# Performance work log

Hardware: AMD Instinct MI355X
Metric: run time of the kernel (lower is better)

Reference implementation:

```python
import jax, jax.numpy as jnp
import numpy as np
import math

EMBED_DIM = 1024
NUM_HEADS = 16
HEAD_DIM = EMBED_DIM // NUM_HEADS


def setup_inputs() -> dict:
    key = jax.random.key(0)
    ks = jax.random.split(key, 11)
    B, S, D = 4, 2048, EMBED_DIM
    scale = 1.0 / math.sqrt(D)
    inp = {
        'q': jax.random.normal(ks[0], (B, S, D), dtype=jnp.float32),
        'k': jax.random.normal(ks[1], (B, S, D), dtype=jnp.float32),
        'v': jax.random.normal(ks[2], (B, S, D), dtype=jnp.float32),
        'Wq': jax.random.normal(ks[3], (D, D), dtype=jnp.float32) * scale,
        'bq': jnp.zeros((D,), dtype=jnp.float32),
        'Wk': jax.random.normal(ks[4], (D, D), dtype=jnp.float32) * scale,
        'bk': jnp.zeros((D,), dtype=jnp.float32),
        'Wv': jax.random.normal(ks[5], (D, D), dtype=jnp.float32) * scale,
        'bv': jnp.zeros((D,), dtype=jnp.float32),
        'Wo': jax.random.normal(ks[6], (D, D), dtype=jnp.float32) * scale,
        'bo': jnp.zeros((D,), dtype=jnp.float32),
    }
    return inp


def reference(q, k, v, Wq, bq, Wk, bk, Wv, bv, Wo, bo):
    B, S, D = q.shape
    H, Hd = NUM_HEADS, HEAD_DIM
    # QKV projections (nn.Linear: x @ W.T + b), split into heads -> [B,H,S,Hd]
    qh = (q @ Wq.T + bq).reshape(B, S, H, Hd).transpose(0, 2, 1, 3)
    kh = (k @ Wk.T + bk).reshape(B, S, H, Hd).transpose(0, 2, 1, 3)
    vh = (v @ Wv.T + bv).reshape(B, S, H, Hd).transpose(0, 2, 1, 3)
    # Scaled dot-product attention, full [B,H,S,S] scores as in source
    scores = jnp.einsum('bhqd,bhkd->bhqk', qh, kh) / math.sqrt(Hd)
    probs = jax.nn.softmax(scores, axis=-1)
    attn = jnp.einsum('bhqk,bhkd->bhqd', probs, vh)
    # Merge heads and output projection
    concat = attn.transpose(0, 2, 1, 3).reshape(B, S, D)
    return concat @ Wo.T + bo
```

## Files before the change

kernel.cpp:

```cpp
#include <hip/hip_runtime.h>
#include <hip/hip_bf16.h>
#include <math.h>

#define D_MODEL 1024
#define NHEADS  16
#define HDIM    64
#define BATCH   4
#define SEQ     2048

typedef __attribute__((ext_vector_type(8))) short short8;
typedef __attribute__((ext_vector_type(4))) float f32x4;

__device__ __forceinline__ short bf16_of(float f) {
  __hip_bfloat16 h = __float2bfloat16(f);
  return *reinterpret_cast<short*>(&h);
}

__device__ __forceinline__ unsigned pack2(float lo, float hi) {
  return (unsigned)(unsigned short)bf16_of(lo) |
         ((unsigned)(unsigned short)bf16_of(hi) << 16);
}

__device__ __forceinline__ unsigned cvtpk(float lo, float hi) {
  unsigned r;
  asm("v_cvt_pk_bf16_f32 %0, %1, %2" : "=v"(r) : "v"(lo), "v"(hi));
  return r;
}

__device__ __forceinline__ short8 mk_frag(unsigned a, unsigned b, unsigned c, unsigned d) {
  union { unsigned u[4]; short8 s; } t;
  t.u[0] = a; t.u[1] = b; t.u[2] = c; t.u[3] = d;
  return t.s;
}

__device__ __forceinline__ float fast_exp2(float x) {
  float r;
  asm("v_exp_f32 %0, %1" : "=v"(r) : "v"(x));
  return r;
}

__device__ __forceinline__ void gload16(const void* g, void* l) {
  __builtin_amdgcn_global_load_lds((const __attribute__((address_space(1))) void*)g,
                                   (__attribute__((address_space(3))) void*)l, 16, 0, 0);
}

__global__ __launch_bounds__(256) void cvt7(
    const float* __restrict__ Wq, const float* __restrict__ Wk,
    const float* __restrict__ Wv, const float* __restrict__ Wo,
    const float* __restrict__ q,  const float* __restrict__ k,
    const float* __restrict__ v,
    short* __restrict__ wdst, short* __restrict__ qc,
    short* __restrict__ kc,   short* __restrict__ vc)
{
  const int w = blockIdx.y;
  const float* s;
  short* d;
  int n4;
  if (w < 4) {
    s = (w == 0) ? Wq : (w == 1) ? Wk : (w == 2) ? Wv : Wo;
    d = wdst + (size_t)w * D_MODEL * D_MODEL;
    n4 = D_MODEL * D_MODEL / 4;
  } else {
    s = (w == 4) ? q : (w == 5) ? k : v;
    d = (w == 4) ? qc : (w == 5) ? kc : vc;
    n4 = BATCH * SEQ * D_MODEL / 4;
  }
  int stride = gridDim.x * blockDim.x;
  for (int i = blockIdx.x * blockDim.x + threadIdx.x; i < n4; i += stride) {
    float4 fv = reinterpret_cast<const float4*>(s)[i];
    reinterpret_cast<uint2*>(d)[i] = make_uint2(pack2(fv.x, fv.y), pack2(fv.z, fv.w));
  }
}

__global__ __launch_bounds__(256) void qkv_gemm(
    const short* __restrict__ qc, const short* __restrict__ kc, const short* __restrict__ vc,
    const short* __restrict__ Wqkv,
    const float* __restrict__ bq, const float* __restrict__ bk, const float* __restrict__ bv,
    short* __restrict__ Qb, short* __restrict__ Kb, short* __restrict__ VTb)
{
  const int tid  = threadIdx.x;
  const int lane = tid & 63;
  const int wave = tid >> 6;
  const int Lb  = blockIdx.x + 24 * blockIdx.y;
  const int xcd = Lb & 7;
  const int sl  = Lb >> 3;
  const int bx  = sl % 24;
  const int by  = (sl / 24) * 8 + xcd;

  const int sel = bx >> 3;
  const short* A    = (sel == 0) ? qc : (sel == 1) ? kc : vc;
  const float* bias = (sel == 0) ? bq : (sel == 1) ? bk : bv;
  const int m0  = by * 128;
  const int n0g = bx * 128;
  const int n0  = n0g & 1023;
  const int wm = (wave >> 1) * 64;
  const int wn = (wave & 1) * 64;

  __shared__ short As[128 * 32];
  __shared__ short Bs[128 * 32];

  f32x4 acc[4][4];
#pragma unroll
  for (int m = 0; m < 4; ++m)
#pragma unroll
    for (int n = 0; n < 4; ++n)
      acc[m][n] = (f32x4){0.f, 0.f, 0.f, 0.f};

  for (int k0 = 0; k0 < D_MODEL; k0 += 32) {
#pragma unroll
    for (int i = 0; i < 2; ++i) {
      int t = i * 256 + wave * 64 + lane;
      int row = t >> 2, c8 = (t & 3) * 8;
      gload16(&A[(size_t)(m0 + row) * D_MODEL + k0 + c8],     &As[i * 2048 + wave * 512]);
      gload16(&Wqkv[(size_t)(n0g + row) * D_MODEL + k0 + c8], &Bs[i * 2048 + wave * 512]);
    }
    __syncthreads();

    short8 afr[4], bfr[4];
#pragma unroll
    for (int m = 0; m < 4; ++m)
      afr[m] = *reinterpret_cast<const short8*>(&As[(wm + m * 16 + (lane & 15)) * 32 + (lane >> 4) * 8]);
#pragma unroll
    for (int n = 0; n < 4; ++n)
      bfr[n] = *reinterpret_cast<const short8*>(&Bs[(wn + n * 16 + (lane & 15)) * 32 + (lane >> 4) * 8]);
#pragma unroll
    for (int m = 0; m < 4; ++m)
#pragma unroll
      for (int n = 0; n < 4; ++n)
        acc[m][n] = __builtin_amdgcn_mfma_f32_16x16x32_bf16(afr[m], bfr[n], acc[m][n], 0, 0, 0);
    __syncthreads();
  }

  if (sel < 2) {
    short* Out = (sel == 0) ? Qb : Kb;
#pragma unroll
    for (int n = 0; n < 4; ++n) {
      int col = n0 + wn + n * 16 + (lane & 15);
      float bval = bias[col];
#pragma unroll
      for (int m = 0; m < 4; ++m) {
        int rowb = m0 + wm + m * 16 + (lane >> 4) * 4;
#pragma unroll
        for (int r = 0; r < 4; ++r)
          Out[(size_t)(rowb + r) * D_MODEL + col] = bf16_of(acc[m][n][r] + bval);
      }
    }
  } else {
#pragma unroll
    for (int n = 0; n < 4; ++n) {
      int col = n0 + wn + n * 16 + (lane & 15);
      float bval = bias[col];
      int h = col >> 6, d = col & 63;
#pragma unroll
      for (int m = 0; m < 4; ++m) {
        int s0 = m0 + wm + m * 16 + (lane >> 4) * 4;
        int b = s0 >> 11, sloc = s0 & 2047;
        unsigned lo = pack2(acc[m][n][0] + bval, acc[m][n][1] + bval);
        unsigned hi = pack2(acc[m][n][2] + bval, acc[m][n][3] + bval);
        *reinterpret_cast<uint2*>(
            &VTb[(((size_t)b * NHEADS + h) * HDIM + d) * SEQ + sloc]) = make_uint2(lo, hi);
      }
    }
  }
}

__global__ __launch_bounds__(256) void gemm_out(
    const short* __restrict__ A, const short* __restrict__ Bw,
    const float* __restrict__ bias, float* __restrict__ Out,
    int M, int N, int K)
{
  const int tid  = threadIdx.x;
  const int lane = tid & 63;
  const int wave = tid >> 6;
  const int Lb  = blockIdx.x + 8 * blockIdx.y;
  const int xcd = Lb & 7;
  const int sl  = Lb >> 3;
  const int bx  = sl & 7;
  const int by  = (sl >> 3) * 8 + xcd;
  const int m0 = by * 128;
  const int n0 = bx * 128;
  const int wm = (wave >> 1) * 64;
  const int wn = (wave & 1) * 64;

  __shared__ short As[128 * 32];
  __shared__ short Bs[128 * 32];

  f32x4 acc[4][4];
#pragma unroll
  for (int m = 0; m < 4; ++m)
#pragma unroll
    for (int n = 0; n < 4; ++n)
      acc[m][n] = (f32x4){0.f, 0.f, 0.f, 0.f};

  for (int k0 = 0; k0 < K; k0 += 32) {
#pragma unroll
    for (int i = 0; i < 2; ++i) {
      int t = i * 256 + wave * 64 + lane;
      int row = t >> 2, c8 = (t & 3) * 8;
      gload16(&A[(size_t)(m0 + row) * K + k0 + c8],  &As[i * 2048 + wave * 512]);
      gload16(&Bw[(size_t)(n0 + row) * K + k0 + c8], &Bs[i * 2048 + wave * 512]);
    }
    __syncthreads();

    short8 afr[4], bfr[4];
#pragma unroll
    for (int m = 0; m < 4; ++m)
      afr[m] = *reinterpret_cast<const short8*>(&As[(wm + m * 16 + (lane & 15)) * 32 + (lane >> 4) * 8]);
#pragma unroll
    for (int n = 0; n < 4; ++n)
      bfr[n] = *reinterpret_cast<const short8*>(&Bs[(wn + n * 16 + (lane & 15)) * 32 + (lane >> 4) * 8]);
#pragma unroll
    for (int m = 0; m < 4; ++m)
#pragma unroll
      for (int n = 0; n < 4; ++n)
        acc[m][n] = __builtin_amdgcn_mfma_f32_16x16x32_bf16(afr[m], bfr[n], acc[m][n], 0, 0, 0);
    __syncthreads();
  }

#pragma unroll
  for (int n = 0; n < 4; ++n) {
    int col = n0 + wn + n * 16 + (lane & 15);
    float bval = bias[col];
#pragma unroll
    for (int m = 0; m < 4; ++m) {
      int rowb = m0 + wm + m * 16 + (lane >> 4) * 4;
#pragma unroll
      for (int r = 0; r < 4; ++r)
        Out[(size_t)(rowb + r) * N + col] = acc[m][n][r] + bval;
    }
  }
}

__global__ __launch_bounds__(512) void attn_fwd(
    const short* __restrict__ Q,
    const short* __restrict__ Kg,
    const short* __restrict__ VT,
    short* __restrict__ Oc)
{
  const int tid = threadIdx.x, lane = tid & 63, wave = tid >> 6;
  const int qi = lane & 15, g = lane >> 4;
  const int Lb  = blockIdx.x + 16 * blockIdx.y;
  const int xcd = Lb & 7;
  const int slot = Lb >> 3;
  const int bh  = (slot >> 4) * 8 + xcd;
  const int qblk = slot & 15;
  const int q0 = qblk * 128;
  const int b = bh >> 4, h = bh & 15;

  __shared__ short Ks[2][64][72];
  __shared__ short Vs[2][64][72];

  const float CEXP = 0.18033688f;
  const float SMC  = 14.4269504f;
  const short8 ones = mk_frag(0x3F803F80u, 0x3F803F80u, 0x3F803F80u, 0x3F803F80u);

  short8 qfr[2];
  {
    int qrow = q0 + wave * 16 + qi;
    const short* qp = &Q[((size_t)b * SEQ + qrow) * D_MODEL + h * HDIM + g * 8];
    qfr[0] = *reinterpret_cast<const short8*>(qp);
    qfr[1] = *reinterpret_cast<const short8*>(qp + 32);
  }

  const size_t kbase = ((size_t)b * SEQ) * D_MODEL + h * HDIM;
  const size_t vbase = ((size_t)bh * HDIM) * SEQ;

  f32x4 o[4], o_l;
#pragma unroll
  for (int db = 0; db < 4; ++db) o[db] = (f32x4){0.f, 0.f, 0.f, 0.f};
  o_l = (f32x4){0.f, 0.f, 0.f, 0.f};

  {
    int row = tid >> 3, sub = tid & 7;
    *reinterpret_cast<uint4*>(&Ks[0][row][sub * 8]) =
        *reinterpret_cast<const uint4*>(&Kg[kbase + (size_t)row * D_MODEL + sub * 8]);
    uint4 vv = *reinterpret_cast<const uint4*>(&VT[vbase + (size_t)row * SEQ + sub * 8]);
    int posA = 32 * (sub >> 2) + 16 * (sub & 1) + 4 * ((sub >> 1) & 1);
    *reinterpret_cast<uint2*>(&Vs[0][row][posA])     = make_uint2(vv.x, vv.y);
    *reinterpret_cast<uint2*>(&Vs[0][row][posA + 8]) = make_uint2(vv.z, vv.w);
  }
  __syncthreads();

  for (int t = 0; t < SEQ / 64; ++t) {
    const int cur = t & 1;
    const bool more = (t + 1) < SEQ / 64;
    const int row = tid >> 3, sub = tid & 7;
    uint4 kreg, vreg;
    if (more) {
      int k0 = (t + 1) * 64;
      kreg = *reinterpret_cast<const uint4*>(&Kg[kbase + (size_t)(k0 + row) * D_MODEL + sub * 8]);
      vreg = *reinterpret_cast<const uint4*>(&VT[vbase + (size_t)row * SEQ + k0 + sub * 8]);
    }

    f32x4 st[4];
    __builtin_amdgcn_s_setprio(1);
#pragma unroll
    for (int n = 0; n < 4; ++n) {
      short8 a0 = *reinterpret_cast<const short8*>(&Ks[cur][n * 16 + qi][g * 8]);
      short8 a1 = *reinterpret_cast<const short8*>(&Ks[cur][n * 16 + qi][32 + g * 8]);
      f32x4 z = (f32x4){0.f, 0.f, 0.f, 0.f};
      z = __builtin_amdgcn_mfma_f32_16x16x32_bf16(a0, qfr[0], z, 0, 0, 0);
      z = __builtin_amdgcn_mfma_f32_16x16x32_bf16(a1, qfr[1], z, 0, 0, 0);
      st[n] = z;
    }
    __builtin_amdgcn_s_setprio(0);

    unsigned pk[4][2];
#pragma unroll
    for (int n = 0; n < 4; ++n) {
#pragma unroll
      for (int r = 0; r < 4; ++r)
        st[n][r] = fast_exp2(fmaf(st[n][r], CEXP, -SMC));
      pk[n][0] = cvtpk(st[n][0], st[n][1]);
      pk[n][1] = cvtpk(st[n][2], st[n][3]);
    }

    short8 pb0 = mk_frag(pk[0][0], pk[0][1], pk[1][0], pk[1][1]);
    short8 pb1 = mk_frag(pk[2][0], pk[2][1], pk[3][0], pk[3][1]);
    __builtin_amdgcn_s_setprio(1);
#pragma unroll
    for (int db = 0; db < 4; ++db) {
      short8 va0 = *reinterpret_cast<const short8*>(&Vs[cur][db * 16 + qi][g * 8]);
      short8 va1 = *reinterpret_cast<const short8*>(&Vs[cur][db * 16 + qi][32 + g * 8]);
      o[db] = __builtin_amdgcn_mfma_f32_16x16x32_bf16(va0, pb0, o[db], 0, 0, 0);
      o[db] = __builtin_amdgcn_mfma_f32_16x16x32_bf16(va1, pb1, o[db], 0, 0, 0);
    }
    o_l = __builtin_amdgcn_mfma_f32_16x16x32_bf16(ones, pb0, o_l, 0, 0, 0);
    o_l = __builtin_amdgcn_mfma_f32_16x16x32_bf16(ones, pb1, o_l, 0, 0, 0);
    __builtin_amdgcn_s_setprio(0);

    if (more) {
      const int nb = cur ^ 1;
      *reinterpret_cast<uint4*>(&Ks[nb][row][sub * 8]) = kreg;
      int posA = 32 * (sub >> 2) + 16 * (sub & 1) + 4 * ((sub >> 1) & 1);
      *reinterpret_cast<uint2*>(&Vs[nb][row][posA])     = make_uint2(vreg.x, vreg.y);
      *reinterpret_cast<uint2*>(&Vs[nb][row][posA + 8]) = make_uint2(vreg.z, vreg.w);
    }

    __syncthreads();
  }

  short (*Os)[72] = reinterpret_cast<short(*)[72]>(&Ks[0][0][0]);
  float inv = 1.f / o_l[0];
#pragma unroll
  for (int db = 0; db < 4; ++db)
#pragma unroll
    for (int r = 0; r < 4; ++r)
      Os[wave * 16 + qi][db * 16 + g * 4 + r] = bf16_of(o[db][r] * inv);
  __syncthreads();
#pragma unroll
  for (int i = 0; i < 2; ++i) {
    int c = tid + i * 512;
    int row = c >> 3, sub = c & 7;
    *reinterpret_cast<uint4*>(&Oc[((size_t)b * SEQ + q0 + row) * D_MODEL + h * HDIM + sub * 8]) =
        *reinterpret_cast<const uint4*>(&Os[row][sub * 8]);
  }
}

extern "C" void kernel_launch(void* const* d_in, const int* in_sizes, int n_in,
                              void* d_out, int out_size, void* d_ws, size_t ws_size,
                              hipStream_t stream)
{
  const float* q  = (const float*)d_in[0];
  const float* k  = (const float*)d_in[1];
  const float* v  = (const float*)d_in[2];
  const float* Wq = (const float*)d_in[3];
  const float* bq = (const float*)d_in[4];
  const float* Wk = (const float*)d_in[5];
  const float* bk = (const float*)d_in[6];
  const float* Wv = (const float*)d_in[7];
  const float* bv = (const float*)d_in[8];
  const float* Wo = (const float*)d_in[9];
  const float* bo = (const float*)d_in[10];

  char* ws = (char*)d_ws;
  const size_t MB = 1ull << 20;
  short* Wqkv_b = (short*)(ws + 0 * MB);
  short* Wo_b   = (short*)(ws + 6 * MB);
  short* Qb     = (short*)(ws + 8 * MB);
  short* Kb     = (short*)(ws + 24 * MB);
  short* VTb    = (short*)(ws + 40 * MB);
  short* qc     = (short*)(ws + 56 * MB);
  short* kc     = (short*)(ws + 72 * MB);
  short* vc     = (short*)(ws + 88 * MB);
  short* Ac     = (short*)(ws + 56 * MB);

  const int M = BATCH * SEQ;

  cvt7<<<dim3(256, 7), 256, 0, stream>>>(Wq, Wk, Wv, Wo, q, k, v, Wqkv_b, qc, kc, vc);

  qkv_gemm<<<dim3(24, M / 128), 256, 0, stream>>>(qc, kc, vc, Wqkv_b, bq, bk, bv, Qb, Kb, VTb);

  attn_fwd<<<dim3(SEQ / 128, BATCH * NHEADS), 512, 0, stream>>>(Qb, Kb, VTb, Ac);

  gemm_out<<<dim3(D_MODEL / 128, M / 128), 256, 0, stream>>>(Ac, Wo_b, bo, (float*)d_out,
                                                             M, D_MODEL, D_MODEL);
}
```

Measured before the change: 222.3 us.

## Process two 16-row query tiles per wave in attention to reuse K/V fragments

Each wave now computes 32 query rows, so each K and V fragment loaded from shared memory feeds two sets of MFMAs. The block covers 256 queries, halving the number of blocks and the K/V global and LDS traffic per query. This raises register pressure, since accumulators and scores are doubled under a 4-waves-per-EU launch bound, and it reduces the number of blocks available for occupancy.

```diff
diff --git a/kernel.cpp b/kernel.cpp
--- a/kernel.cpp
+++ b/kernel.cpp
@@ -231,7 +231,7 @@
   }
 }
 
-__global__ __launch_bounds__(512) void attn_fwd(
+__global__ __launch_bounds__(512, 4) void attn_fwd(
     const short* __restrict__ Q,
     const short* __restrict__ Kg,
     const short* __restrict__ VT,
@@ -239,122 +239,143 @@
 {
   const int tid = threadIdx.x, lane = tid & 63, wave = tid >> 6;
   const int qi = lane & 15, g = lane >> 4;
-  const int Lb  = blockIdx.x + 16 * blockIdx.y;
+  const int Lb  = blockIdx.x + 8 * blockIdx.y;
   const int xcd = Lb & 7;
   const int slot = Lb >> 3;
-  const int bh  = (slot >> 4) * 8 + xcd;
-  const int qblk = slot & 15;
-  const int q0 = qblk * 128;
+  const int bh  = (slot >> 3) * 8 + xcd;
+  const int q0  = (slot & 7) * 256;
   const int b = bh >> 4, h = bh & 15;
 
-  __shared__ short Ks[2][64][72];
-  __shared__ short Vs[2][64][72];
+  __shared__ short SH[18432];
+#define KS(buf, row, col) SH[(buf) * 4608 + (row) * 72 + (col)]
+#define VS(buf, row, col) SH[9216 + (buf) * 4608 + (row) * 72 + (col)]
 
   const float CEXP = 0.18033688f;
   const float SMC  = 14.4269504f;
   const short8 ones = mk_frag(0x3F803F80u, 0x3F803F80u, 0x3F803F80u, 0x3F803F80u);
 
-  short8 qfr[2];
-  {
-    int qrow = q0 + wave * 16 + qi;
+  short8 qfr[2][2];
+#pragma unroll
+  for (int L = 0; L < 2; ++L) {
+    int qrow = q0 + wave * 32 + L * 16 + qi;
     const short* qp = &Q[((size_t)b * SEQ + qrow) * D_MODEL + h * HDIM + g * 8];
-    qfr[0] = *reinterpret_cast<const short8*>(qp);
-    qfr[1] = *reinterpret_cast<const short8*>(qp + 32);
+    qfr[L][0] = *reinterpret_cast<const short8*>(qp);
+    qfr[L][1] = *reinterpret_cast<const short8*>(qp + 32);
   }
 
   const size_t kbase = ((size_t)b * SEQ) * D_MODEL + h * HDIM;
   const size_t vbase = ((size_t)bh * HDIM) * SEQ;
 
-  f32x4 o[4], o_l;
-#pragma unroll
-  for (int db = 0; db < 4; ++db) o[db] = (f32x4){0.f, 0.f, 0.f, 0.f};
-  o_l = (f32x4){0.f, 0.f, 0.f, 0.f};
+  f32x4 o[2][4], o_l[2];
+#pragma unroll
+  for (int L = 0; L < 2; ++L) {
+    o_l[L] = (f32x4){0.f, 0.f, 0.f, 0.f};
+#pragma unroll
+    for (int db = 0; db < 4; ++db) o[L][db] = (f32x4){0.f, 0.f, 0.f, 0.f};
+  }
+
+  const int srow = tid >> 3, ssub = tid & 7;
+  const int posA = 32 * (ssub >> 2) + 16 * (ssub & 1) + 4 * ((ssub >> 1) & 1);
 
   {
-    int row = tid >> 3, sub = tid & 7;
-    *reinterpret_cast<uint4*>(&Ks[0][row][sub * 8]) =
-        *reinterpret_cast<const uint4*>(&Kg[kbase + (size_t)row * D_MODEL + sub * 8]);
-    uint4 vv = *reinterpret_cast<const uint4*>(&VT[vbase + (size_t)row * SEQ + sub * 8]);
-    int posA = 32 * (sub >> 2) + 16 * (sub & 1) + 4 * ((sub >> 1) & 1);
-    *reinterpret_cast<uint2*>(&Vs[0][row][posA])     = make_uint2(vv.x, vv.y);
-    *reinterpret_cast<uint2*>(&Vs[0][row][posA + 8]) = make_uint2(vv.z, vv.w);
+    *reinterpret_cast<uint4*>(&KS(0, srow, ssub * 8)) =
+        *reinterpret_cast<const uint4*>(&Kg[kbase + (size_t)srow * D_MODEL + ssub * 8]);
+    uint4 vv = *reinterpret_cast<const uint4*>(&VT[vbase + (size_t)srow * SEQ + ssub * 8]);
+    *reinterpret_cast<uint2*>(&VS(0, srow, posA))     = make_uint2(vv.x, vv.y);
+    *reinterpret_cast<uint2*>(&VS(0, srow, posA + 8)) = make_uint2(vv.z, vv.w);
   }
   __syncthreads();
 
   for (int t = 0; t < SEQ / 64; ++t) {
     const int cur = t & 1;
     const bool more = (t + 1) < SEQ / 64;
-    const int row = tid >> 3, sub = tid & 7;
     uint4 kreg, vreg;
     if (more) {
       int k0 = (t + 1) * 64;
-      kreg = *reinterpret_cast<const uint4*>(&Kg[kbase + (size_t)(k0 + row) * D_MODEL + sub * 8]);
-      vreg = *reinterpret_cast<const uint4*>(&VT[vbase + (size_t)row * SEQ + k0 + sub * 8]);
-    }
-
-    f32x4 st[4];
+      kreg = *reinterpret_cast<const uint4*>(&Kg[kbase + (size_t)(k0 + srow) * D_MODEL + ssub * 8]);
+      vreg = *reinterpret_cast<const uint4*>(&VT[vbase + (size_t)srow * SEQ + k0 + ssub * 8]);
+    }
+
+    f32x4 st[2][4];
     __builtin_amdgcn_s_setprio(1);
 #pragma unroll
     for (int n = 0; n < 4; ++n) {
-      short8 a0 = *reinterpret_cast<const short8*>(&Ks[cur][n * 16 + qi][g * 8]);
-      short8 a1 = *reinterpret_cast<const short8*>(&Ks[cur][n * 16 + qi][32 + g * 8]);
-      f32x4 z = (f32x4){0.f, 0.f, 0.f, 0.f};
-      z = __builtin_amdgcn_mfma_f32_16x16x32_bf16(a0, qfr[0], z, 0, 0, 0);
-      z = __builtin_amdgcn_mfma_f32_16x16x32_bf16(a1, qfr[1], z, 0, 0, 0);
-      st[n] = z;
+      short8 a0 = *reinterpret_cast<const short8*>(&KS(cur, n * 16 + qi, g * 8));
+      short8 a1 = *reinterpret_cast<const short8*>(&KS(cur, n * 16 + qi, 32 + g * 8));
+#pragma unroll
+      for (int L = 0; L < 2; ++L) {
+        f32x4 z = (f32x4){0.f, 0.f, 0.f, 0.f};
+        z = __builtin_amdgcn_mfma_f32_16x16x32_bf16(a0, qfr[L][0], z, 0, 0, 0);
+        z = __builtin_amdgcn_mfma_f32_16x16x32_bf16(a1, qfr[L][1], z, 0, 0, 0);
+        st[L][n] = z;
+      }
     }
     __builtin_amdgcn_s_setprio(0);
 
-    unsigned pk[4][2];
-#pragma unroll
-    for (int n = 0; n < 4; ++n) {
-#pragma unroll
-      for (int r = 0; r < 4; ++r)
-        st[n][r] = fast_exp2(fmaf(st[n][r], CEXP, -SMC));
-      pk[n][0] = cvtpk(st[n][0], st[n][1]);
-      pk[n][1] = cvtpk(st[n][2], st[n][3]);
-    }
-
-    short8 pb0 = mk_frag(pk[0][0], pk[0][1], pk[1][0], pk[1][1]);
-    short8 pb1 = mk_frag(pk[2][0], pk[2][1], pk[3][0], pk[3][1]);
+    short8 pb[2][2];
+#pragma unroll
+    for (int L = 0; L < 2; ++L) {
+      unsigned pk[4][2];
+#pragma unroll
+      for (int n = 0; n < 4; ++n) {
+#pragma unroll
+        for (int r = 0; r < 4; ++r)
+          st[L][n][r] = fast_exp2(fmaf(st[L][n][r], CEXP, -SMC));
+        pk[n][0] = cvtpk(st[L][n][0], st[L][n][1]);
+        pk[n][1] = cvtpk(st[L][n][2], st[L][n][3]);
+      }
+      pb[L][0] = mk_frag(pk[0][0], pk[0][1], pk[1][0], pk[1][1]);
+      pb[L][1] = mk_frag(pk[2][0], pk[2][1], pk[3][0], pk[3][1]);
+    }
+
     __builtin_amdgcn_s_setprio(1);
 #pragma unroll
     for (int db = 0; db < 4; ++db) {
-      short8 va0 = *reinterpret_cast<const short8*>(&Vs[cur][db * 16 + qi][g * 8]);
-      short8 va1 = *reinterpret_cast<const short8*>(&Vs[cur][db * 16 + qi][32 + g * 8]);
-      o[db] = __builtin_amdgcn_mfma_f32_16x16x32_bf16(va0, pb0, o[db], 0, 0, 0);
-      o[db] = __builtin_amdgcn_mfma_f32_16x16x32_bf16(va1, pb1, o[db], 0, 0, 0);
-    }
-    o_l = __builtin_amdgcn_mfma_f32_16x16x32_bf16(ones, pb0, o_l, 0, 0, 0);
-    o_l = __builtin_amdgcn_mfma_f32_16x16x32_bf16(ones, pb1, o_l, 0, 0, 0);
+      short8 va0 = *reinterpret_cast<const short8*>(&VS(cur, db * 16 + qi, g * 8));
+      short8 va1 = *reinterpret_cast<const short8*>(&VS(cur, db * 16 + qi, 32 + g * 8));
+#pragma unroll
+      for (int L = 0; L < 2; ++L) {
+        o[L][db] = __builtin_amdgcn_mfma_f32_16x16x32_bf16(va0, pb[L][0], o[L][db], 0, 0, 0);
+        o[L][db] = __builtin_amdgcn_mfma_f32_16x16x32_bf16(va1, pb[L][1], o[L][db], 0, 0, 0);
+      }
+    }
+#pragma unroll
+    for (int L = 0; L < 2; ++L) {
+      o_l[L] = __builtin_amdgcn_mfma_f32_16x16x32_bf16(ones, pb[L][0], o_l[L], 0, 0, 0);
+      o_l[L] = __builtin_amdgcn_mfma_f32_16x16x32_bf16(ones, pb[L][1], o_l[L], 0, 0, 0);
+    }
     __builtin_amdgcn_s_setprio(0);
 
     if (more) {
       const int nb = cur ^ 1;
-      *reinterpret_cast<uint4*>(&Ks[nb][row][sub * 8]) = kreg;
-      int posA = 32 * (sub >> 2) + 16 * (sub & 1) + 4 * ((sub >> 1) & 1);
-      *reinterpret_cast<uint2*>(&Vs[nb][row][posA])     = make_uint2(vreg.x, vreg.y);
-      *reinterpret_cast<uint2*>(&Vs[nb][row][posA + 8]) = make_uint2(vreg.z, vreg.w);
+      *reinterpret_cast<uint4*>(&KS(nb, srow, ssub * 8)) = kreg;
+      *reinterpret_cast<uint2*>(&VS(nb, srow, posA))     = make_uint2(vreg.x, vreg.y);
+      *reinterpret_cast<uint2*>(&VS(nb, srow, posA + 8)) = make_uint2(vreg.z, vreg.w);
     }
 
     __syncthreads();
   }
 
-  short (*Os)[72] = reinterpret_cast<short(*)[72]>(&Ks[0][0][0]);
-  float inv = 1.f / o_l[0];
-#pragma unroll
-  for (int db = 0; db < 4; ++db)
-#pragma unroll
-    for (int r = 0; r < 4; ++r)
-      Os[wave * 16 + qi][db * 16 + g * 4 + r] = bf16_of(o[db][r] * inv);
+  short (*Os)[72] = reinterpret_cast<short(*)[72]>(&SH[0]);
+#pragma unroll
+  for (int L = 0; L < 2; ++L) {
+    float inv = 1.f / o_l[L][0];
+#pragma unroll
+    for (int db = 0; db < 4; ++db)
+#pragma unroll
+      for (int r = 0; r < 4; ++r)
+        Os[wave * 32 + L * 16 + qi][db * 16 + g * 4 + r] = bf16_of(o[L][db][r] * inv);
+  }
   __syncthreads();
 #pragma unroll
-  for (int i = 0; i < 2; ++i) {
+  for (int i = 0; i < 4; ++i) {
     int c = tid + i * 512;
     int row = c >> 3, sub = c & 7;
     *reinterpret_cast<uint4*>(&Oc[((size_t)b * SEQ + q0 + row) * D_MODEL + h * HDIM + sub * 8]) =
         *reinterpret_cast<const uint4*>(&Os[row][sub * 8]);
   }
+#undef KS
+#undef VS
 }
 
 extern "C" void kernel_launch(void* const* d_in, const int* in_sizes, int n_in,
@@ -391,7 +412,7 @@
 
   qkv_gemm<<<dim3(24, M / 128), 256, 0, stream>>>(qc, kc, vc, Wqkv_b, bq, bk, bv, Qb, Kb, VTb);
 
-  attn_fwd<<<dim3(SEQ / 128, BATCH * NHEADS), 512, 0, stream>>>(Qb, Kb, VTb, Ac);
+  attn_fwd<<<dim3(SEQ / 256, BATCH * NHEADS), 512, 0, stream>>>(Qb, Kb, VTb, Ac);
 
   gemm_out<<<dim3(D_MODEL / 128, M / 128), 256, 0, stream>>>(Ac, Wo_b, bo, (float*)d_out,
                                                              M, D_MODEL, D_MODEL);
```

Result: faster. 204.9 us (-7.8%).
